# Performance work log

Hardware: AMD Instinct MI355X
Metric: run time of the kernel (lower is better)

Reference implementation:

```python
import jax, jax.numpy as jnp
import numpy as np

B, T, C, NH = 4, 2048, 1024, 16
HS = C // NH


def setup_inputs() -> dict:
    key = jax.random.key(0)
    k1, k2, k3, k4, k5 = jax.random.split(key, 5)
    s = 1.0 / np.sqrt(C)
    return {
        "x": jax.random.normal(k1, (B, T, C), dtype=jnp.float32),
        "Wqkv": jax.random.normal(k2, (3 * C, C), dtype=jnp.float32) * s,
        "bqkv": jax.random.normal(k3, (3 * C,), dtype=jnp.float32) * 0.02,
        "Wproj": jax.random.normal(k4, (C, C), dtype=jnp.float32) * s,
        "bproj": jax.random.normal(k5, (C,), dtype=jnp.float32) * 0.02,
    }


def reference(x, Wqkv, bqkv, Wproj, bproj):
    Bsz, Tlen, Cdim = x.shape
    # qkv projection (torch Linear: x @ W.T + b)
    qkv = x @ Wqkv.T + bqkv                      # [B, T, 3C]
    q, k, v = jnp.split(qkv, 3, axis=-1)
    # [B, NH, T, HS]
    q = q.reshape(Bsz, Tlen, NH, HS).transpose(0, 2, 1, 3)
    k = k.reshape(Bsz, Tlen, NH, HS).transpose(0, 2, 1, 3)
    v = v.reshape(Bsz, Tlen, NH, HS).transpose(0, 2, 1, 3)
    scale = 1.0 / np.sqrt(HS)
    att = jnp.einsum('bhqd,bhkd->bhqk', q, k) * scale
    causal = jnp.triu(jnp.ones((Tlen, Tlen), dtype=bool), k=1)
    att = jnp.where(causal[None, None], -jnp.inf, att)
    att = jax.nn.softmax(att, axis=-1)
    y = jnp.einsum('bhqk,bhkd->bhqd', att, v)    # [B, NH, T, HS]
    y = y.transpose(0, 2, 1, 3).reshape(Bsz, Tlen, Cdim)
    return y @ Wproj.T + bproj
```

## Files before the change

### kernel.cpp

```cpp
#include <hip/hip_runtime.h>
#include <hip/hip_bf16.h>

#define B_   4
#define T_   2048
#define C_   1024
#define NH_  16
#define HS_  64
#define M_   8192
#define N1_  3072
#define BH_  64

typedef __attribute__((ext_vector_type(8))) short short8;
typedef __attribute__((ext_vector_type(4))) short short4v;
typedef __attribute__((ext_vector_type(4))) float f32x4;

__device__ __forceinline__ short f2bf(float f) {
  unsigned u = __float_as_uint(f);
  unsigned r = (u + 0x7fffu + ((u >> 16) & 1u)) >> 16;
  return (short)r;
}
__device__ __forceinline__ unsigned pk_bf16(float a, float b) {
  __hip_bfloat162 h = __float22bfloat162_rn(make_float2(a, b));
  union { __hip_bfloat162 h2; unsigned u; } cv; cv.h2 = h; return cv.u;
}

typedef __attribute__((address_space(1))) unsigned int as1_uint;
typedef __attribute__((address_space(3))) unsigned int as3_uint;
__device__ __forceinline__ void g2l16(const void* g, void* l) {
  __builtin_amdgcn_global_load_lds((as1_uint*)g, (as3_uint*)l, 16, 0, 0);
}

__global__ __launch_bounds__(256) void conv_bf16(
    const float* __restrict__ src, short* __restrict__ dst)
{
  const size_t i = ((size_t)blockIdx.x * 256 + threadIdx.x) * 8;
  const f32x4 a = *(const f32x4*)&src[i];
  const f32x4 b = *(const f32x4*)&src[i + 4];
  short8 o;
  o[0] = f2bf(a[0]); o[1] = f2bf(a[1]); o[2] = f2bf(a[2]); o[3] = f2bf(a[3]);
  o[4] = f2bf(b[0]); o[5] = f2bf(b[1]); o[6] = f2bf(b[2]); o[7] = f2bf(b[3]);
  *(short8*)&dst[i] = o;
}

__global__ __launch_bounds__(256) void qkv_gemm(
    const short* __restrict__ X,
    const short* __restrict__ W,
    const float* __restrict__ bias,
    short* __restrict__ Qo, short* __restrict__ Ko, short* __restrict__ Vt)
{
  __shared__ short As[2][128 * 64];
  __shared__ short Bs[2][128 * 64];
  const int tid = threadIdx.x;
  const int lane = tid & 63;
  const int wid = tid >> 6;
  const int wy = wid >> 1, wx = wid & 1;
  const int lq = lane >> 4, lm = lane & 15;
  const int row0 = blockIdx.x * 128;
  const int col0 = blockIdx.y * 128;

  f32x4 acc[4][4] = {};

  const int ar = tid >> 3;
  const int ac = (tid & 7) << 3;

#pragma unroll
  for (int j = 0; j < 4; ++j) {
    const int r = ar + j * 32;
    g2l16(&X[(size_t)(row0 + r) * C_ + ac], &As[0][r * 64 + ac]);
    g2l16(&W[(size_t)(col0 + r) * C_ + ac], &Bs[0][r * 64 + ac]);
  }
  __syncthreads();

  int cur = 0;
  for (int k0 = 0; k0 < C_; k0 += 64) {
    if (k0 + 64 < C_) {
#pragma unroll
      for (int j = 0; j < 4; ++j) {
        const int r = ar + j * 32;
        g2l16(&X[(size_t)(row0 + r) * C_ + k0 + 64 + ac], &As[cur ^ 1][r * 64 + ac]);
        g2l16(&W[(size_t)(col0 + r) * C_ + k0 + 64 + ac], &Bs[cur ^ 1][r * 64 + ac]);
      }
    }

#pragma unroll
    for (int kk = 0; kk < 2; ++kk) {
      short8 af[4], bfr[4];
#pragma unroll
      for (int mi = 0; mi < 4; ++mi)
        af[mi] = *(const short8*)&As[cur][(wy * 64 + mi * 16 + lm) * 64 + kk * 32 + lq * 8];
#pragma unroll
      for (int ni = 0; ni < 4; ++ni)
        bfr[ni] = *(const short8*)&Bs[cur][(wx * 64 + ni * 16 + lm) * 64 + kk * 32 + lq * 8];
#pragma unroll
      for (int mi = 0; mi < 4; ++mi)
#pragma unroll
        for (int ni = 0; ni < 4; ++ni)
          acc[mi][ni] = __builtin_amdgcn_mfma_f32_16x16x32_bf16(af[mi], bfr[ni], acc[mi][ni], 0, 0, 0);
    }

    __syncthreads();
    cur ^= 1;
  }

#pragma unroll
  for (int ni = 0; ni < 4; ++ni) {
    const int n = col0 + wx * 64 + ni * 16 + lm;
    const float bv = bias[n];
    const int sel = n >> 10;
    const int cc = n & (C_ - 1);
    const int h = cc >> 6, d = cc & 63;
    if (sel == 2) {
#pragma unroll
      for (int mi = 0; mi < 4; ++mi) {
        const int m0 = row0 + wy * 64 + mi * 16 + lq * 4;
        const int b = m0 >> 11, t0 = m0 & (T_ - 1);
        const int bh = b * NH_ + h;
        short4v o;
#pragma unroll
        for (int i = 0; i < 4; ++i) o[i] = f2bf(acc[mi][ni][i] + bv);
        *(short4v*)&Vt[((size_t)bh * HS_ + d) * T_ + t0] = o;
      }
    } else {
      short* dst = (sel == 0) ? Qo : Ko;
#pragma unroll
      for (int mi = 0; mi < 4; ++mi) {
#pragma unroll
        for (int i = 0; i < 4; ++i) {
          const int m = row0 + wy * 64 + mi * 16 + lq * 4 + i;
          const int b = m >> 11, t = m & (T_ - 1);
          const int bh = b * NH_ + h;
          dst[((size_t)bh * T_ + t) * HS_ + d] = f2bf(acc[mi][ni][i] + bv);
        }
      }
    }
  }
}

__global__ __launch_bounds__(256) void proj_gemm(
    const short* __restrict__ Y,
    const short* __restrict__ W,
    const float* __restrict__ bias,
    float* __restrict__ Out)
{
  __shared__ short As[2][128 * 64];
  __shared__ short Bs[2][128 * 64];
  const int tid = threadIdx.x;
  const int lane = tid & 63;
  const int wid = tid >> 6;
  const int wy = wid >> 1, wx = wid & 1;
  const int lq = lane >> 4, lm = lane & 15;
  const int row0 = blockIdx.x * 128;
  const int col0 = blockIdx.y * 128;

  f32x4 acc[4][4] = {};

  const int ar = tid >> 3;
  const int ac = (tid & 7) << 3;

#pragma unroll
  for (int j = 0; j < 4; ++j) {
    const int r = ar + j * 32;
    g2l16(&Y[(size_t)(row0 + r) * C_ + ac], &As[0][r * 64 + ac]);
    g2l16(&W[(size_t)(col0 + r) * C_ + ac], &Bs[0][r * 64 + ac]);
  }
  __syncthreads();

  int cur = 0;
  for (int k0 = 0; k0 < C_; k0 += 64) {
    if (k0 + 64 < C_) {
#pragma unroll
      for (int j = 0; j < 4; ++j) {
        const int r = ar + j * 32;
        g2l16(&Y[(size_t)(row0 + r) * C_ + k0 + 64 + ac], &As[cur ^ 1][r * 64 + ac]);
        g2l16(&W[(size_t)(col0 + r) * C_ + k0 + 64 + ac], &Bs[cur ^ 1][r * 64 + ac]);
      }
    }

#pragma unroll
    for (int kk = 0; kk < 2; ++kk) {
      short8 af[4], bfr[4];
#pragma unroll
      for (int mi = 0; mi < 4; ++mi)
        af[mi] = *(const short8*)&As[cur][(wy * 64 + mi * 16 + lm) * 64 + kk * 32 + lq * 8];
#pragma unroll
      for (int ni = 0; ni < 4; ++ni)
        bfr[ni] = *(const short8*)&Bs[cur][(wx * 64 + ni * 16 + lm) * 64 + kk * 32 + lq * 8];
#pragma unroll
      for (int mi = 0; mi < 4; ++mi)
#pragma unroll
        for (int ni = 0; ni < 4; ++ni)
          acc[mi][ni] = __builtin_amdgcn_mfma_f32_16x16x32_bf16(af[mi], bfr[ni], acc[mi][ni], 0, 0, 0);
    }

    __syncthreads();
    cur ^= 1;
  }

#pragma unroll
  for (int ni = 0; ni < 4; ++ni) {
    const int n = col0 + wx * 64 + ni * 16 + lm;
    const float bv = bias[n];
#pragma unroll
    for (int mi = 0; mi < 4; ++mi) {
#pragma unroll
      for (int i = 0; i < 4; ++i) {
        const int m = row0 + wy * 64 + mi * 16 + lq * 4 + i;
        Out[(size_t)m * C_ + n] = acc[mi][ni][i] + bv;
      }
    }
  }
}

#define LDK 72
__global__ __launch_bounds__(256) void attn(
    const short* __restrict__ Qg, const short* __restrict__ Kg,
    const short* __restrict__ Vg, short* __restrict__ Yo)
{
  __shared__ short Ks[64 * LDK];
  __shared__ short Vs[64 * LDK];

  const int tid = threadIdx.x;
  const int lane = tid & 63;
  const int w = tid >> 6;
  const int lq = lane >> 4, lm = lane & 15;
  const int bh = blockIdx.y;
  const int b = bh >> 4, h = bh & 15;
  const size_t base = (size_t)bh * T_ * HS_;
  const short* __restrict__ Kb = Kg + base;
  const short* __restrict__ Vb = Vg + base;
  const float sf = 0.125f * 1.44269504089f;

  const int sr = tid >> 3;
  const int sc = (tid & 7) * 8;

#pragma unroll 1
  for (int half = 0; half < 2; ++half) {
    const int qt = half ? (int)blockIdx.x : 31 - (int)blockIdx.x;
    const int q0 = qt * 64;
    const int q = q0 + w * 16 + lm;

    const short8 qf0 = *(const short8*)&Qg[base + (size_t)q * HS_ + lq * 8];
    const short8 qf1 = *(const short8*)&Qg[base + (size_t)q * HS_ + 32 + lq * 8];

    float l_part = 0.0f;
    f32x4 o_acc[4] = {};

    short8 pk0 = *(const short8*)&Kb[(size_t)sr * HS_ + sc];
    short8 pk1 = *(const short8*)&Kb[(size_t)(32 + sr) * HS_ + sc];
    short8 pv0 = *(const short8*)&Vb[(size_t)sr * T_ + sc];
    short8 pv1 = *(const short8*)&Vb[(size_t)(32 + sr) * T_ + sc];

#pragma unroll 1
    for (int kt = 0; kt <= qt; ++kt) {
      const int kv0 = kt * 64;

      __syncthreads();
      *(short8*)&Ks[sr * LDK + sc] = pk0;
      *(short8*)&Ks[(32 + sr) * LDK + sc] = pk1;
      *(short8*)&Vs[sr * LDK + sc] = pv0;
      *(short8*)&Vs[(32 + sr) * LDK + sc] = pv1;
      __syncthreads();

      if (kt < qt) {
        const int nk = kv0 + 64;
        pk0 = *(const short8*)&Kb[(size_t)(nk + sr) * HS_ + sc];
        pk1 = *(const short8*)&Kb[(size_t)(nk + 32 + sr) * HS_ + sc];
        pv0 = *(const short8*)&Vb[(size_t)sr * T_ + nk + sc];
        pv1 = *(const short8*)&Vb[(size_t)(32 + sr) * T_ + nk + sc];
      }

      f32x4 sv[4];
#pragma unroll
      for (int ni = 0; ni < 4; ++ni) {
        const short8 kf0 = *(const short8*)&Ks[(ni * 16 + lm) * LDK + lq * 8];
        const short8 kf1 = *(const short8*)&Ks[(ni * 16 + lm) * LDK + 32 + lq * 8];
        f32x4 s = {};
        s = __builtin_amdgcn_mfma_f32_16x16x32_bf16(kf0, qf0, s, 0, 0, 0);
        sv[ni] = __builtin_amdgcn_mfma_f32_16x16x32_bf16(kf1, qf1, s, 0, 0, 0);
      }

      if (kt == qt) {
#pragma unroll
        for (int ni = 0; ni < 4; ++ni) {
          const int kvb = kv0 + ni * 16 + lq * 4;
#pragma unroll
          for (int i = 0; i < 4; ++i)
            if (kvb + i > q) sv[ni][i] = -3.0e38f;
        }
      }

#pragma unroll
      for (int ni = 0; ni < 4; ++ni)
#pragma unroll
        for (int i = 0; i < 4; ++i)
          sv[ni][i] = __builtin_amdgcn_exp2f(sv[ni][i] * sf);

      l_part += ((sv[0][0] + sv[0][1]) + (sv[0][2] + sv[0][3]))
              + ((sv[1][0] + sv[1][1]) + (sv[1][2] + sv[1][3]))
              + ((sv[2][0] + sv[2][1]) + (sv[2][2] + sv[2][3]))
              + ((sv[3][0] + sv[3][1]) + (sv[3][2] + sv[3][3]));

      short4v p4[4];
#pragma unroll
      for (int ni = 0; ni < 4; ++ni) {
        union { short4v s4; unsigned u[2]; } pk;
        pk.u[0] = pk_bf16(sv[ni][0], sv[ni][1]);
        pk.u[1] = pk_bf16(sv[ni][2], sv[ni][3]);
        p4[ni] = pk.s4;
      }

#pragma unroll
      for (int di = 0; di < 4; ++di) {
#pragma unroll
        for (int ni = 0; ni < 4; ++ni) {
          const short4v vfr = *(const short4v*)&Vs[(di * 16 + lm) * LDK + ni * 16 + lq * 4];
          o_acc[di] = __builtin_amdgcn_mfma_f32_16x16x16bf16_1k(vfr, p4[ni], o_acc[di], 0, 0, 0);
        }
      }
    }

    float l = l_part;
    l += __shfl_xor(l, 16);
    l += __shfl_xor(l, 32);
    const float rl = 1.0f / l;
    const size_t rowo = ((size_t)(b * T_ + q)) * C_ + h * HS_;
#pragma unroll
    for (int di = 0; di < 4; ++di) {
      union { short4v s4; unsigned u[2]; } pk;
      pk.u[0] = pk_bf16(o_acc[di][0] * rl, o_acc[di][1] * rl);
      pk.u[1] = pk_bf16(o_acc[di][2] * rl, o_acc[di][3] * rl);
      *(short4v*)&Yo[rowo + di * 16 + lq * 4] = pk.s4;
    }
  }
}

extern "C" void kernel_launch(void* const* d_in, const int* in_sizes, int n_in,
                              void* d_out, int out_size, void* d_ws, size_t ws_size,
                              hipStream_t stream) {
  (void)in_sizes; (void)n_in; (void)out_size;
  const float* x     = (const float*)d_in[0];
  const float* Wqkv  = (const float*)d_in[1];
  const float* bqkv  = (const float*)d_in[2];
  const float* Wproj = (const float*)d_in[3];
  const float* bproj = (const float*)d_in[4];
  float* out = (float*)d_out;

  const size_t nWq = (size_t)N1_ * C_;
  const size_t nWp = (size_t)C_ * C_;
  const size_t nFull = (size_t)M_ * C_;
  const size_t nB = (size_t)T_ * C_;

  dim3 blk(256);
  const size_t need_batched = (nWq + nWp + 4 * nFull) * sizeof(short);

  if (ws_size >= need_batched) {
    short* Wq_bf = (short*)d_ws;
    short* Wp_bf = Wq_bf + nWq;
    short* S0    = Wp_bf + nWp;
    short* Qw    = S0 + nFull;
    short* Kw    = Qw + nFull;
    short* Vw    = Kw + nFull;

    conv_bf16<<<dim3((int)(nWq / 2048)), blk, 0, stream>>>(Wqkv, Wq_bf);
    conv_bf16<<<dim3((int)(nWp / 2048)), blk, 0, stream>>>(Wproj, Wp_bf);
    conv_bf16<<<dim3((int)(nFull / 2048)), blk, 0, stream>>>(x, S0);
    qkv_gemm<<<dim3(M_ / 128, N1_ / 128), blk, 0, stream>>>(S0, Wq_bf, bqkv, Qw, Kw, Vw);
    attn<<<dim3(16, BH_), blk, 0, stream>>>(Qw, Kw, Vw, S0);
    proj_gemm<<<dim3(M_ / 128, C_ / 128), blk, 0, stream>>>(S0, Wp_bf, bproj, out);
  } else {
    short* Wq_bf = (short*)d_ws;
    short* Wp_bf = Wq_bf + nWq;
    short* S0    = Wp_bf + nWp;
    short* Qw    = S0 + nB;
    short* Kw    = Qw + nB;
    short* Vw    = Kw + nB;

    conv_bf16<<<dim3((int)(nWq / 2048)), blk, 0, stream>>>(Wqkv, Wq_bf);
    conv_bf16<<<dim3((int)(nWp / 2048)), blk, 0, stream>>>(Wproj, Wp_bf);
    for (int b = 0; b < B_; ++b) {
      const float* xb = x   + (size_t)b * nB;
      float*       ob = out + (size_t)b * nB;
      conv_bf16<<<dim3((int)(nB / 2048)), blk, 0, stream>>>(xb, S0);
      qkv_gemm<<<dim3(T_ / 128, N1_ / 128), blk, 0, stream>>>(S0, Wq_bf, bqkv, Qw, Kw, Vw);
      attn<<<dim3(16, NH_), blk, 0, stream>>>(Qw, Kw, Vw, S0);
      proj_gemm<<<dim3(T_ / 128, C_ / 128), blk, 0, stream>>>(S0, Wp_bf, bproj, ob);
    }
  }
}
```

Before: 272.7 us.

## Load K fragments directly from global into registers and prescale Q

The attention kernel no longer stages K tiles through shared memory. Each wave loads its K MFMA fragments straight from global memory into registers and prefetches the next tile after the QK MFMAs. Separately, the softmax scale times log2(e) is folded into Q when the QKV GEMM writes it out, which removes a multiply per score. The cost is that all four waves now read the same K tile redundantly from global or L2 rather than sharing one LDS copy, register pressure rises, and rounding Q to bf16 after scaling changes numerics slightly.

```diff
diff --git a/kernel.cpp b/kernel.cpp
--- a/kernel.cpp
+++ b/kernel.cpp
@@ -13,6 +13,8 @@
 typedef __attribute__((ext_vector_type(8))) short short8;
 typedef __attribute__((ext_vector_type(4))) short short4v;
 typedef __attribute__((ext_vector_type(4))) float f32x4;
+
+#define QSCALE 0.18033688011112042f
 
 __device__ __forceinline__ short f2bf(float f) {
   unsigned u = __float_as_uint(f);
@@ -122,6 +124,7 @@
       }
     } else {
       short* dst = (sel == 0) ? Qo : Ko;
+      const float qs = (sel == 0) ? QSCALE : 1.0f;
 #pragma unroll
       for (int mi = 0; mi < 4; ++mi) {
 #pragma unroll
@@ -129,7 +132,7 @@
           const int m = row0 + wy * 64 + mi * 16 + lq * 4 + i;
           const int b = m >> 11, t = m & (T_ - 1);
           const int bh = b * NH_ + h;
-          dst[((size_t)bh * T_ + t) * HS_ + d] = f2bf(acc[mi][ni][i] + bv);
+          dst[((size_t)bh * T_ + t) * HS_ + d] = f2bf((acc[mi][ni][i] + bv) * qs);
         }
       }
     }
@@ -216,7 +219,6 @@
     const short* __restrict__ Qg, const short* __restrict__ Kg,
     const short* __restrict__ Vg, short* __restrict__ Yo)
 {
-  __shared__ short Ks[64 * LDK];
   __shared__ short Vs[64 * LDK];
 
   const int tid = threadIdx.x;
@@ -228,16 +230,15 @@
   const size_t base = (size_t)bh * T_ * HS_;
   const short* __restrict__ Kb = Kg + base;
   const short* __restrict__ Vb = Vg + base;
-  const float sf = 0.125f * 1.44269504089f;
 
   const int sr = tid >> 3;
   const int sc = (tid & 7) * 8;
+  const int kroff = lm * HS_ + lq * 8;
 
 #pragma unroll 1
   for (int half = 0; half < 2; ++half) {
     const int qt = half ? (int)blockIdx.x : 31 - (int)blockIdx.x;
-    const int q0 = qt * 64;
-    const int q = q0 + w * 16 + lm;
+    const int q = qt * 64 + w * 16 + lm;
 
     const short8 qf0 = *(const short8*)&Qg[base + (size_t)q * HS_ + lq * 8];
     const short8 qf1 = *(const short8*)&Qg[base + (size_t)q * HS_ + 32 + lq * 8];
@@ -245,8 +246,13 @@
     float l_part = 0.0f;
     f32x4 o_acc[4] = {};
 
-    short8 pk0 = *(const short8*)&Kb[(size_t)sr * HS_ + sc];
-    short8 pk1 = *(const short8*)&Kb[(size_t)(32 + sr) * HS_ + sc];
+    short8 kf[8];
+#pragma unroll
+    for (int ni = 0; ni < 4; ++ni) {
+      kf[2 * ni]     = *(const short8*)&Kb[(size_t)(ni * 16) * HS_ + kroff];
+      kf[2 * ni + 1] = *(const short8*)&Kb[(size_t)(ni * 16) * HS_ + 32 + kroff];
+    }
+
     short8 pv0 = *(const short8*)&Vb[(size_t)sr * T_ + sc];
     short8 pv1 = *(const short8*)&Vb[(size_t)(32 + sr) * T_ + sc];
 
@@ -255,16 +261,12 @@
       const int kv0 = kt * 64;
 
       __syncthreads();
-      *(short8*)&Ks[sr * LDK + sc] = pk0;
-      *(short8*)&Ks[(32 + sr) * LDK + sc] = pk1;
       *(short8*)&Vs[sr * LDK + sc] = pv0;
       *(short8*)&Vs[(32 + sr) * LDK + sc] = pv1;
       __syncthreads();
 
       if (kt < qt) {
         const int nk = kv0 + 64;
-        pk0 = *(const short8*)&Kb[(size_t)(nk + sr) * HS_ + sc];
-        pk1 = *(const short8*)&Kb[(size_t)(nk + 32 + sr) * HS_ + sc];
         pv0 = *(const short8*)&Vb[(size_t)sr * T_ + nk + sc];
         pv1 = *(const short8*)&Vb[(size_t)(32 + sr) * T_ + nk + sc];
       }
@@ -272,11 +274,18 @@
       f32x4 sv[4];
 #pragma unroll
       for (int ni = 0; ni < 4; ++ni) {
-        const short8 kf0 = *(const short8*)&Ks[(ni * 16 + lm) * LDK + lq * 8];
-        const short8 kf1 = *(const short8*)&Ks[(ni * 16 + lm) * LDK + 32 + lq * 8];
         f32x4 s = {};
-        s = __builtin_amdgcn_mfma_f32_16x16x32_bf16(kf0, qf0, s, 0, 0, 0);
-        sv[ni] = __builtin_amdgcn_mfma_f32_16x16x32_bf16(kf1, qf1, s, 0, 0, 0);
+        s = __builtin_amdgcn_mfma_f32_16x16x32_bf16(kf[2 * ni], qf0, s, 0, 0, 0);
+        sv[ni] = __builtin_amdgcn_mfma_f32_16x16x32_bf16(kf[2 * ni + 1], qf1, s, 0, 0, 0);
+      }
+
+      if (kt < qt) {
+        const short* Ktn = Kb + (size_t)(kv0 + 64) * HS_;
+#pragma unroll
+        for (int ni = 0; ni < 4; ++ni) {
+          kf[2 * ni]     = *(const short8*)&Ktn[(ni * 16) * HS_ + kroff];
+          kf[2 * ni + 1] = *(const short8*)&Ktn[(ni * 16) * HS_ + 32 + kroff];
+        }
       }
 
       if (kt == qt) {
@@ -293,7 +302,7 @@
       for (int ni = 0; ni < 4; ++ni)
 #pragma unroll
         for (int i = 0; i < 4; ++i)
-          sv[ni][i] = __builtin_amdgcn_exp2f(sv[ni][i] * sf);
+          sv[ni][i] = __builtin_amdgcn_exp2f(sv[ni][i]);
 
       l_part += ((sv[0][0] + sv[0][1]) + (sv[0][2] + sv[0][3]))
               + ((sv[1][0] + sv[1][1]) + (sv[1][2] + sv[1][3]))
```

Measured after the change: 331.8 us. 21.7% more time.
